# Optimization experiments

Hardware: AMD Instinct MI355X
Metric: run time of the kernel (lower is better)

The kernel has to match this reference:

```python
import jax, jax.numpy as jnp
import numpy as np

N_USER = 200000
N_TITEM = 200000  # sized >= N_USER because original code indexes ti_emb with user ids (faithful to source bug)
D = 256           # embed_dim
H = 128           # hidden = embed_dim // 2
N_HID = 2         # config.layers - 1 extra hidden blocks
B = 65536


def setup_inputs() -> dict:
    key = jax.random.key(0)
    ks = jax.random.split(key, 10)
    sc_d = 1.0 / np.sqrt(D)
    sc_h = 1.0 / np.sqrt(H)
    return {
        "user": jax.random.randint(ks[0], (B,), 0, N_USER),
        "item": jax.random.randint(ks[1], (B,), 0, 100000),
        "su_table": jax.random.normal(ks[2], (N_USER, D), jnp.float32) * 0.1,
        "ti_table": jax.random.normal(ks[3], (N_TITEM, D), jnp.float32) * 0.1,
        # 3 parallel MLP towers, stacked on leading axis t=3
        "Win": jax.random.normal(ks[4], (3, D, H), jnp.float32) * sc_d,
        "bin_": jnp.zeros((3, H), jnp.float32),
        "Wh": jax.random.normal(ks[5], (3, N_HID, H, H), jnp.float32) * sc_h,
        "bh": jnp.zeros((3, N_HID, H), jnp.float32),
        "Wout": jax.random.normal(ks[6], (3, H, D), jnp.float32) * sc_h,
        "bout": jnp.zeros((3, D), jnp.float32),
    }


def _towers(u, Win, bin_, Wh, bh, Wout, bout):
    # u: [B, D] -> x: [3, B, D] (three structurally identical MLP towers, batched)
    h = jax.nn.relu(jnp.einsum("bd,tdh->tbh", u, Win) + bin_[:, None, :])
    for i in range(N_HID):  # fixed small layer count
        h = jax.nn.relu(jnp.einsum("tbh,thk->tbk", h, Wh[:, i]) + bh[:, i][:, None, :])
    return jnp.einsum("tbh,thd->tbd", h, Wout) + bout[:, None, :]


def reference(user, item, su_table, ti_table, Win, bin_, Wh, bh, Wout, bout):
    u_embed = su_table[user]            # [B, D]
    i_key = ti_table[user]              # [B, D]  (faithful: original indexes ti_emb with `user`)
    x = _towers(u_embed, Win, bin_, Wh, bh, Wout, bout)   # [3, B, D]
    logits = jnp.einsum("tbd,bd->bt", x, i_key)           # [B, 3]
    attn = jax.nn.softmax(logits, axis=1)                 # [B, 3]
    fu = jnp.einsum("bt,tbd->bd", attn, x)                # [B, D]
    i_embed = ti_table[item]                              # [B, D]
    score = jnp.sum(fu * i_embed, axis=1)                 # [B]
    return score
```

## Files before the change

kernel.cpp:

```cpp
#include <hip/hip_runtime.h>
#include <hip/hip_bf16.h>
#include <stdint.h>

typedef __attribute__((ext_vector_type(8))) short short8;
typedef __attribute__((ext_vector_type(4))) float f32x4;

__device__ __forceinline__ short f2bf(float f) {
  __hip_bfloat16 h = __float2bfloat16(f);
  union { __hip_bfloat16 h; unsigned short u; } c;
  c.h = h;
  return (short)c.u;
}
__device__ __forceinline__ short8 cvt8(const float* p) {
  const float4 f0 = *(const float4*)p;
  const float4 f1 = *(const float4*)(p + 4);
  short8 r;
  r[0] = f2bf(f0.x); r[1] = f2bf(f0.y); r[2] = f2bf(f0.z); r[3] = f2bf(f0.w);
  r[4] = f2bf(f1.x); r[5] = f2bf(f1.y); r[6] = f2bf(f1.z); r[7] = f2bf(f1.w);
  return r;
}

__global__ __launch_bounds__(256) void pack_weights(
    const float* __restrict__ Win, const float* __restrict__ Wh,
    const float* __restrict__ Wout, short* __restrict__ o) {
  int gid = blockIdx.x * 256 + threadIdx.x;
  if (gid < 12288) {
    int t = gid / 4096, r = gid % 4096;
    int ks = r / 512, r2 = r % 512, nf = r2 / 64, l = r2 % 64;
    int n = nf * 16 + (l & 15);
    int kb = ks * 32 + (l >> 4) * 8;
#pragma unroll
    for (int i = 0; i < 8; ++i)
      o[gid * 8 + i] = f2bf(Win[(t * 256 + kb + i) * 128 + n]);
  } else if (gid < 24576) {
    int h = gid - 12288;
    int tl = h / 2048, r = h % 2048;
    int ks = r / 512, nf = (r % 512) / 64, l = r % 64;
    int n = nf * 16 + (l & 15);
    int kb = ks * 32 + (l >> 4) * 8;
#pragma unroll
    for (int i = 0; i < 8; ++i)
      o[98304 + h * 8 + i] = f2bf(Wh[(tl * 128 + kb + i) * 128 + n]);
  } else {
    int oo = gid - 24576;
    int t = oo / 4096, r = oo % 4096;
    int ks = r / 1024, nf = (r % 1024) / 64, l = r % 64;
    int n = nf * 16 + (l & 15);
    int kb = ks * 32 + (l >> 4) * 8;
#pragma unroll
    for (int i = 0; i < 8; ++i)
      o[196608 + oo * 8 + i] = f2bf(Wout[(t * 128 + kb + i) * 256 + n]);
  }
}

__device__ __forceinline__ void stageN(const short* __restrict__ wp, char* lbuf,
                                       int pageBase, int tid, int rounds) {
  const char* g = (const char*)wp + (size_t)pageBase * 1024 + (size_t)tid * 16;
  char* l = lbuf + (tid >> 6) * 1024;
  for (int r = 0; r < rounds; ++r) {
    __builtin_amdgcn_global_load_lds(
        (const __attribute__((address_space(1))) void*)(g + r * 4096),
        (__attribute__((address_space(3))) void*)(l + r * 4096), 16, 0, 0);
  }
}

__global__ __launch_bounds__(256) void k_gather_u(
    const int* __restrict__ user, const float* __restrict__ su,
    short* __restrict__ U, int nrows) {
  const int idx = blockIdx.x * 256 + threadIdx.x;
  const int row = idx >> 5, c = idx & 31;
  const int uid = user[row];
  *(short8*)(U + (size_t)row * 256 + c * 8) = cvt8(su + (size_t)uid * 256 + c * 8);
}

__global__ __launch_bounds__(256, 2) void k_l1(
    const short* __restrict__ U, const float* __restrict__ bin,
    const short* __restrict__ wp, short* __restrict__ H1, int nrows) {
  __shared__ __align__(16) char sB[65536];
  const int tid = threadIdx.x, w = tid >> 6, lane = tid & 63;
  const int ar = lane & 15, g = lane >> 4;
  const int t = blockIdx.y;
  const int rblk = blockIdx.x * 128;
  const f32x4 fz = {0.f, 0.f, 0.f, 0.f};

  stageN(wp, sB, t * 64, tid, 16);
  __syncthreads();

  f32x4 acc[8][2];
#pragma unroll
  for (int m = 0; m < 8; ++m) { acc[m][0] = fz; acc[m][1] = fz; }
#pragma unroll
  for (int K0 = 0; K0 < 8; ++K0) {
    short8 a[8];
#pragma unroll
    for (int m = 0; m < 8; ++m)
      a[m] = *(const short8*)(U + (size_t)(rblk + m * 16 + ar) * 256 + K0 * 32 + g * 8);
#pragma unroll
    for (int nfl = 0; nfl < 2; ++nfl) {
      const short8 b = *(const short8*)(sB + (K0 * 8 + w * 2 + nfl) * 1024 + lane * 16);
#pragma unroll
      for (int m = 0; m < 8; ++m)
        acc[m][nfl] = __builtin_amdgcn_mfma_f32_16x16x32_bf16(a[m], b, acc[m][nfl], 0, 0, 0);
    }
  }
#pragma unroll
  for (int m = 0; m < 8; ++m)
#pragma unroll
    for (int nfl = 0; nfl < 2; ++nfl) {
      const int col = w * 32 + nfl * 16 + ar;
      const float bv = bin[t * 128 + col];
#pragma unroll
      for (int q = 0; q < 4; ++q) {
        const int r = rblk + m * 16 + g * 4 + q;
        H1[((size_t)t * nrows + r) * 128 + col] = f2bf(fmaxf(acc[m][nfl][q] + bv, 0.f));
      }
    }
}

__global__ __launch_bounds__(256, 2) void k_l23(
    const short* __restrict__ H1, const float* __restrict__ bh,
    const short* __restrict__ wp, short* __restrict__ H3, int nrows) {
  __shared__ __align__(16) char sB[65536];
  __shared__ __align__(16) char H2[16384];
  const int tid = threadIdx.x, w = tid >> 6, lane = tid & 63;
  const int ar = lane & 15, g = lane >> 4;
  const int t = blockIdx.y;
  const int rblk = blockIdx.x * 64;
  const int swzA = (ar & 7) << 4;
  const f32x4 fz = {0.f, 0.f, 0.f, 0.f};

  stageN(wp, sB, 192 + t * 64, tid, 16);
  __syncthreads();

  f32x4 acc[4][2];
#pragma unroll
  for (int m = 0; m < 4; ++m) { acc[m][0] = fz; acc[m][1] = fz; }
#pragma unroll
  for (int ks = 0; ks < 4; ++ks) {
    short8 a[4];
#pragma unroll
    for (int m = 0; m < 4; ++m)
      a[m] = *(const short8*)(H1 + ((size_t)t * nrows + rblk + m * 16 + ar) * 128 + ks * 32 + g * 8);
#pragma unroll
    for (int nfl = 0; nfl < 2; ++nfl) {
      const short8 b = *(const short8*)(sB + (ks * 8 + w * 2 + nfl) * 1024 + lane * 16);
#pragma unroll
      for (int m = 0; m < 4; ++m)
        acc[m][nfl] = __builtin_amdgcn_mfma_f32_16x16x32_bf16(a[m], b, acc[m][nfl], 0, 0, 0);
    }
  }
#pragma unroll
  for (int m = 0; m < 4; ++m)
#pragma unroll
    for (int nfl = 0; nfl < 2; ++nfl) {
      const int col = w * 32 + nfl * 16 + ar;
      const float bv = bh[(t * 2) * 128 + col];
#pragma unroll
      for (int q = 0; q < 4; ++q) {
        const int r = m * 16 + g * 4 + q;
        *(short*)(H2 + r * 256 + ((col * 2) ^ ((r & 7) << 4))) =
            f2bf(fmaxf(acc[m][nfl][q] + bv, 0.f));
      }
    }
  __syncthreads();

#pragma unroll
  for (int m = 0; m < 4; ++m) { acc[m][0] = fz; acc[m][1] = fz; }
#pragma unroll
  for (int ks = 0; ks < 4; ++ks) {
    short8 a[4];
#pragma unroll
    for (int m = 0; m < 4; ++m)
      a[m] = *(const short8*)(H2 + (m * 16 + ar) * 256 + ((ks * 64 + g * 16) ^ swzA));
#pragma unroll
    for (int nfl = 0; nfl < 2; ++nfl) {
      const short8 b = *(const short8*)(sB + (32 + ks * 8 + w * 2 + nfl) * 1024 + lane * 16);
#pragma unroll
      for (int m = 0; m < 4; ++m)
        acc[m][nfl] = __builtin_amdgcn_mfma_f32_16x16x32_bf16(a[m], b, acc[m][nfl], 0, 0, 0);
    }
  }
#pragma unroll
  for (int m = 0; m < 4; ++m)
#pragma unroll
    for (int nfl = 0; nfl < 2; ++nfl) {
      const int col = w * 32 + nfl * 16 + ar;
      const float bv = bh[(t * 2 + 1) * 128 + col];
#pragma unroll
      for (int q = 0; q < 4; ++q) {
        const int r = rblk + m * 16 + g * 4 + q;
        H3[((size_t)t * nrows + r) * 128 + col] = f2bf(fmaxf(acc[m][nfl][q] + bv, 0.f));
      }
    }
}

__global__ __launch_bounds__(256, 2) void k_l4tail(
    const short* __restrict__ H3, const float* __restrict__ bout,
    const short* __restrict__ wp, const float* __restrict__ ti,
    const int* __restrict__ user, const int* __restrict__ item,
    float* __restrict__ out, int nrows) {
  __shared__ __align__(16) char WB[2][32768];
  __shared__ float sL[3][64];
  __shared__ float sS[3][64];
  __shared__ int sUid[64];
  __shared__ int sItm[64];
  const int tid = threadIdx.x, w = tid >> 6, lane = tid & 63;
  const int ar = lane & 15, g = lane >> 4;
  const int rblk = blockIdx.x * 64;
  const f32x4 fz = {0.f, 0.f, 0.f, 0.f};

  if (tid < 64) {
    sUid[tid] = user[rblk + tid];
    sItm[tid] = item[rblk + tid];
  }
  if (tid < 192) { (&sL[0][0])[tid] = 0.f; (&sS[0][0])[tid] = 0.f; }
  stageN(wp, WB[0], 384, tid, 8);
  __syncthreads();
  int cur = 0;

  for (int t = 0; t < 3; ++t) {
    f32x4 acc4[4][4];
#pragma unroll
    for (int m = 0; m < 4; ++m)
#pragma unroll
      for (int n = 0; n < 4; ++n) acc4[m][n] = fz;

    for (int half = 0; half < 2; ++half) {
      const int phase = t * 2 + half;
      if (phase < 5) stageN(wp, WB[cur ^ 1], 384 + (phase + 1) * 32, tid, 8);
      const char* wb = WB[cur];
#pragma unroll
      for (int k2 = 0; k2 < 2; ++k2) {
        const int K0 = half * 2 + k2;
        short8 a[4];
#pragma unroll
        for (int m = 0; m < 4; ++m)
          a[m] = *(const short8*)(H3 + ((size_t)t * nrows + rblk + m * 16 + ar) * 128 + K0 * 32 + g * 8);
#pragma unroll
        for (int nfl = 0; nfl < 4; ++nfl) {
          const short8 b = *(const short8*)(wb + (k2 * 16 + w * 4 + nfl) * 1024 + lane * 16);
#pragma unroll
          for (int m = 0; m < 4; ++m)
            acc4[m][nfl] = __builtin_amdgcn_mfma_f32_16x16x32_bf16(a[m], b, acc4[m][nfl], 0, 0, 0);
        }
      }

      if (half == 1) {
        float pl[16], ps[16];
#pragma unroll
        for (int i = 0; i < 16; ++i) { pl[i] = 0.f; ps[i] = 0.f; }
#pragma unroll
        for (int m = 0; m < 4; ++m)
#pragma unroll
          for (int nfl = 0; nfl < 4; ++nfl) {
            const int col = w * 64 + nfl * 16 + ar;
            const float bo = bout[t * 256 + col];
#pragma unroll
            for (int q = 0; q < 4; ++q) {
              const int r = m * 16 + g * 4 + q;
              const float x = acc4[m][nfl][q] + bo;
              pl[m * 4 + q] += x * ti[(size_t)sUid[r] * 256 + col];
              ps[m * 4 + q] += x * ti[(size_t)sItm[r] * 256 + col];
            }
          }
#pragma unroll
        for (int i = 0; i < 16; ++i) {
          float a0 = pl[i], b0 = ps[i];
#pragma unroll
          for (int off = 1; off < 16; off <<= 1) {
            a0 += __shfl_xor(a0, off);
            b0 += __shfl_xor(b0, off);
          }
          pl[i] = a0; ps[i] = b0;
        }
        if (ar == 0) {
#pragma unroll
          for (int m = 0; m < 4; ++m)
#pragma unroll
            for (int q = 0; q < 4; ++q) {
              const int r = m * 16 + g * 4 + q;
              atomicAdd(&sL[t][r], pl[m * 4 + q]);
              atomicAdd(&sS[t][r], ps[m * 4 + q]);
            }
        }
      }
      __syncthreads();
      cur ^= 1;
    }
  }

  if (tid < 64) {
    const float l0 = sL[0][tid], l1 = sL[1][tid], l2 = sL[2][tid];
    const float mx = fmaxf(l0, fmaxf(l1, l2));
    const float e0 = __expf(l0 - mx), e1 = __expf(l1 - mx), e2 = __expf(l2 - mx);
    out[rblk + tid] =
        (e0 * sS[0][tid] + e1 * sS[1][tid] + e2 * sS[2][tid]) / (e0 + e1 + e2);
  }
}

extern "C" void kernel_launch(void* const* d_in, const int* in_sizes, int n_in,
                              void* d_out, int out_size, void* d_ws, size_t ws_size,
                              hipStream_t stream) {
  const int* user = (const int*)d_in[0];
  const int* item = (const int*)d_in[1];
  const float* su = (const float*)d_in[2];
  const float* ti = (const float*)d_in[3];
  const float* Win = (const float*)d_in[4];
  const float* bin = (const float*)d_in[5];
  const float* Wh = (const float*)d_in[6];
  const float* bh = (const float*)d_in[7];
  const float* Wout = (const float*)d_in[8];
  const float* bout = (const float*)d_in[9];
  float* out = (float*)d_out;
  char* ws = (char*)d_ws;

  const size_t WOFF = 1179648;
  short* wpk = (short*)ws;
  hipLaunchKernelGGL(pack_weights, dim3(144), dim3(256), 0, stream, Win, Wh, Wout, wpk);

  size_t avail = (ws_size > WOFF) ? (ws_size - WOFF) : 0;
  long rpc = (long)((avail / 2048) & ~(size_t)127);
  if (rpc > 65536) rpc = 65536;
  if (rpc < 128) rpc = 128;

  short* U = (short*)(ws + WOFF);
  short* H1 = (short*)(ws + WOFF + (size_t)rpc * 512);
  short* H3 = (short*)(ws + WOFF + (size_t)rpc * 512 + (size_t)rpc * 768);

  for (long r0 = 0; r0 < 65536; r0 += rpc) {
    const int nr = (int)((65536 - r0 < rpc) ? (65536 - r0) : rpc);
    hipLaunchKernelGGL(k_gather_u, dim3(nr / 8), dim3(256), 0, stream,
                       user + r0, su, U, nr);
    hipLaunchKernelGGL(k_l1, dim3(nr / 128, 3), dim3(256), 0, stream,
                       U, bin, wpk, H1, nr);
    hipLaunchKernelGGL(k_l23, dim3(nr / 64, 3), dim3(256), 0, stream,
                       H1, bh, wpk, H3, nr);
    hipLaunchKernelGGL(k_l4tail, dim3(nr / 64), dim3(256), 0, stream,
                       H3, bout, wpk, ti, user + r0, item + r0, out + r0, nr);
  }
}
```

Measured before the change: 204.7 us.

## Use persistent grid-stride GEMM kernels and split the output layer from the attention tail

The layer kernels become persistent, capped at 170 blocks per tower, and loop over row tiles, so each block stages its 64KB weight slice into LDS once and reuses it. k_l23 is restructured so each wave owns 16 rows with a private LDS slab, which removes the block-wide barrier between layers 2 and 3. The fused l4+tail kernel is split into a per-tower output GEMM that writes bf16 X to a workspace, followed by a separate vectorized tail kernel that does the ti gathers, dot products and softmax. This adds a [3,B,256] bf16 intermediate round-trip through global memory, and the larger per-row footprint may lower rows per chunk when workspace is small.

```diff
diff --git a/kernel.cpp b/kernel.cpp
--- a/kernel.cpp
+++ b/kernel.cpp
@@ -10,6 +10,10 @@
   union { __hip_bfloat16 h; unsigned short u; } c;
   c.h = h;
   return (short)c.u;
+}
+__device__ __forceinline__ float bf2f(short s) {
+  union { unsigned u; float f; } x; x.u = ((unsigned)(unsigned short)s) << 16;
+  return x.f;
 }
 __device__ __forceinline__ short8 cvt8(const float* p) {
   const float4 f0 = *(const float4*)p;
@@ -80,41 +84,44 @@
   const int tid = threadIdx.x, w = tid >> 6, lane = tid & 63;
   const int ar = lane & 15, g = lane >> 4;
   const int t = blockIdx.y;
-  const int rblk = blockIdx.x * 128;
   const f32x4 fz = {0.f, 0.f, 0.f, 0.f};
 
   stageN(wp, sB, t * 64, tid, 16);
   __syncthreads();
 
-  f32x4 acc[8][2];
-#pragma unroll
-  for (int m = 0; m < 8; ++m) { acc[m][0] = fz; acc[m][1] = fz; }
-#pragma unroll
-  for (int K0 = 0; K0 < 8; ++K0) {
-    short8 a[8];
+  const int ntile = nrows >> 7;
+  for (int tile = blockIdx.x; tile < ntile; tile += gridDim.x) {
+    const int rblk = tile << 7;
+    f32x4 acc[8][2];
+#pragma unroll
+    for (int m = 0; m < 8; ++m) { acc[m][0] = fz; acc[m][1] = fz; }
+#pragma unroll
+    for (int K0 = 0; K0 < 8; ++K0) {
+      short8 a[8];
+#pragma unroll
+      for (int m = 0; m < 8; ++m)
+        a[m] = *(const short8*)(U + (size_t)(rblk + m * 16 + ar) * 256 + K0 * 32 + g * 8);
+#pragma unroll
+      for (int nfl = 0; nfl < 2; ++nfl) {
+        const short8 b = *(const short8*)(sB + (K0 * 8 + w * 2 + nfl) * 1024 + lane * 16);
+#pragma unroll
+        for (int m = 0; m < 8; ++m)
+          acc[m][nfl] = __builtin_amdgcn_mfma_f32_16x16x32_bf16(a[m], b, acc[m][nfl], 0, 0, 0);
+      }
+    }
 #pragma unroll
     for (int m = 0; m < 8; ++m)
-      a[m] = *(const short8*)(U + (size_t)(rblk + m * 16 + ar) * 256 + K0 * 32 + g * 8);
-#pragma unroll
-    for (int nfl = 0; nfl < 2; ++nfl) {
-      const short8 b = *(const short8*)(sB + (K0 * 8 + w * 2 + nfl) * 1024 + lane * 16);
-#pragma unroll
-      for (int m = 0; m < 8; ++m)
-        acc[m][nfl] = __builtin_amdgcn_mfma_f32_16x16x32_bf16(a[m], b, acc[m][nfl], 0, 0, 0);
-    }
-  }
-#pragma unroll
-  for (int m = 0; m < 8; ++m)
-#pragma unroll
-    for (int nfl = 0; nfl < 2; ++nfl) {
-      const int col = w * 32 + nfl * 16 + ar;
-      const float bv = bin[t * 128 + col];
-#pragma unroll
-      for (int q = 0; q < 4; ++q) {
-        const int r = rblk + m * 16 + g * 4 + q;
-        H1[((size_t)t * nrows + r) * 128 + col] = f2bf(fmaxf(acc[m][nfl][q] + bv, 0.f));
-      }
-    }
+#pragma unroll
+      for (int nfl = 0; nfl < 2; ++nfl) {
+        const int col = w * 32 + nfl * 16 + ar;
+        const float bv = bin[t * 128 + col];
+#pragma unroll
+        for (int q = 0; q < 4; ++q) {
+          const int r = rblk + m * 16 + g * 4 + q;
+          H1[((size_t)t * nrows + r) * 128 + col] = f2bf(fmaxf(acc[m][nfl][q] + bv, 0.f));
+        }
+      }
+  }
 }
 
 __global__ __launch_bounds__(256, 2) void k_l23(
@@ -125,176 +132,150 @@
   const int tid = threadIdx.x, w = tid >> 6, lane = tid & 63;
   const int ar = lane & 15, g = lane >> 4;
   const int t = blockIdx.y;
-  const int rblk = blockIdx.x * 64;
   const int swzA = (ar & 7) << 4;
   const f32x4 fz = {0.f, 0.f, 0.f, 0.f};
 
   stageN(wp, sB, 192 + t * 64, tid, 16);
   __syncthreads();
 
-  f32x4 acc[4][2];
-#pragma unroll
-  for (int m = 0; m < 4; ++m) { acc[m][0] = fz; acc[m][1] = fz; }
-#pragma unroll
-  for (int ks = 0; ks < 4; ++ks) {
-    short8 a[4];
-#pragma unroll
-    for (int m = 0; m < 4; ++m)
-      a[m] = *(const short8*)(H1 + ((size_t)t * nrows + rblk + m * 16 + ar) * 128 + ks * 32 + g * 8);
-#pragma unroll
-    for (int nfl = 0; nfl < 2; ++nfl) {
-      const short8 b = *(const short8*)(sB + (ks * 8 + w * 2 + nfl) * 1024 + lane * 16);
-#pragma unroll
-      for (int m = 0; m < 4; ++m)
-        acc[m][nfl] = __builtin_amdgcn_mfma_f32_16x16x32_bf16(a[m], b, acc[m][nfl], 0, 0, 0);
-    }
-  }
-#pragma unroll
-  for (int m = 0; m < 4; ++m)
-#pragma unroll
-    for (int nfl = 0; nfl < 2; ++nfl) {
-      const int col = w * 32 + nfl * 16 + ar;
+  char* const h2 = H2 + w * 4096;
+  const int ntile = nrows >> 6;
+  for (int tile = blockIdx.x; tile < ntile; tile += gridDim.x) {
+    const int base = tile * 64 + w * 16;
+    f32x4 acc[8];
+#pragma unroll
+    for (int nf = 0; nf < 8; ++nf) acc[nf] = fz;
+#pragma unroll
+    for (int ks = 0; ks < 4; ++ks) {
+      const short8 a = *(const short8*)(H1 + ((size_t)t * nrows + base + ar) * 128 + ks * 32 + g * 8);
+#pragma unroll
+      for (int nf = 0; nf < 8; ++nf) {
+        const short8 b = *(const short8*)(sB + (ks * 8 + nf) * 1024 + lane * 16);
+        acc[nf] = __builtin_amdgcn_mfma_f32_16x16x32_bf16(a, b, acc[nf], 0, 0, 0);
+      }
+    }
+#pragma unroll
+    for (int nf = 0; nf < 8; ++nf) {
+      const int col = nf * 16 + ar;
       const float bv = bh[(t * 2) * 128 + col];
 #pragma unroll
       for (int q = 0; q < 4; ++q) {
-        const int r = m * 16 + g * 4 + q;
-        *(short*)(H2 + r * 256 + ((col * 2) ^ ((r & 7) << 4))) =
-            f2bf(fmaxf(acc[m][nfl][q] + bv, 0.f));
-      }
-    }
+        const int r = g * 4 + q;
+        *(short*)(h2 + r * 256 + ((col * 2) ^ ((r & 7) << 4))) =
+            f2bf(fmaxf(acc[nf][q] + bv, 0.f));
+      }
+    }
+#pragma unroll
+    for (int nf = 0; nf < 8; ++nf) acc[nf] = fz;
+#pragma unroll
+    for (int ks = 0; ks < 4; ++ks) {
+      const short8 a = *(const short8*)(h2 + ar * 256 + ((ks * 64 + g * 16) ^ swzA));
+#pragma unroll
+      for (int nf = 0; nf < 8; ++nf) {
+        const short8 b = *(const short8*)(sB + (32 + ks * 8 + nf) * 1024 + lane * 16);
+        acc[nf] = __builtin_amdgcn_mfma_f32_16x16x32_bf16(a, b, acc[nf], 0, 0, 0);
+      }
+    }
+#pragma unroll
+    for (int nf = 0; nf < 8; ++nf) {
+      const int col = nf * 16 + ar;
+      const float bv = bh[(t * 2 + 1) * 128 + col];
+#pragma unroll
+      for (int q = 0; q < 4; ++q) {
+        const int r = base + g * 4 + q;
+        H3[((size_t)t * nrows + r) * 128 + col] = f2bf(fmaxf(acc[nf][q] + bv, 0.f));
+      }
+    }
+  }
+}
+
+__global__ __launch_bounds__(256, 2) void k_l4(
+    const short* __restrict__ H3, const float* __restrict__ bout,
+    const short* __restrict__ wp, short* __restrict__ X, int nrows) {
+  __shared__ __align__(16) char sB[65536];
+  const int tid = threadIdx.x, w = tid >> 6, lane = tid & 63;
+  const int ar = lane & 15, g = lane >> 4;
+  const int t = blockIdx.y;
+  const f32x4 fz = {0.f, 0.f, 0.f, 0.f};
+
+  stageN(wp, sB, 384 + t * 64, tid, 16);
   __syncthreads();
 
-#pragma unroll
-  for (int m = 0; m < 4; ++m) { acc[m][0] = fz; acc[m][1] = fz; }
-#pragma unroll
-  for (int ks = 0; ks < 4; ++ks) {
-    short8 a[4];
-#pragma unroll
-    for (int m = 0; m < 4; ++m)
-      a[m] = *(const short8*)(H2 + (m * 16 + ar) * 256 + ((ks * 64 + g * 16) ^ swzA));
-#pragma unroll
-    for (int nfl = 0; nfl < 2; ++nfl) {
-      const short8 b = *(const short8*)(sB + (32 + ks * 8 + w * 2 + nfl) * 1024 + lane * 16);
-#pragma unroll
-      for (int m = 0; m < 4; ++m)
-        acc[m][nfl] = __builtin_amdgcn_mfma_f32_16x16x32_bf16(a[m], b, acc[m][nfl], 0, 0, 0);
-    }
-  }
-#pragma unroll
-  for (int m = 0; m < 4; ++m)
-#pragma unroll
-    for (int nfl = 0; nfl < 2; ++nfl) {
-      const int col = w * 32 + nfl * 16 + ar;
-      const float bv = bh[(t * 2 + 1) * 128 + col];
+  float bo[16];
+#pragma unroll
+  for (int nf = 0; nf < 16; ++nf) bo[nf] = bout[t * 256 + nf * 16 + ar];
+
+  const int ntile = nrows >> 6;
+  for (int tile = blockIdx.x; tile < ntile; tile += gridDim.x) {
+    const int base = tile * 64 + w * 16;
+    short8 a4[4];
+#pragma unroll
+    for (int K0 = 0; K0 < 4; ++K0)
+      a4[K0] = *(const short8*)(H3 + ((size_t)t * nrows + base + ar) * 128 + K0 * 32 + g * 8);
+    f32x4 acc[16];
+#pragma unroll
+    for (int nf = 0; nf < 16; ++nf) acc[nf] = fz;
+#pragma unroll
+    for (int K0 = 0; K0 < 4; ++K0)
+#pragma unroll
+      for (int nf = 0; nf < 16; ++nf) {
+        const short8 b = *(const short8*)(sB + (K0 * 16 + nf) * 1024 + lane * 16);
+        acc[nf] = __builtin_amdgcn_mfma_f32_16x16x32_bf16(a4[K0], b, acc[nf], 0, 0, 0);
+      }
+#pragma unroll
+    for (int nf = 0; nf < 16; ++nf) {
+      const int col = nf * 16 + ar;
 #pragma unroll
       for (int q = 0; q < 4; ++q) {
-        const int r = rblk + m * 16 + g * 4 + q;
-        H3[((size_t)t * nrows + r) * 128 + col] = f2bf(fmaxf(acc[m][nfl][q] + bv, 0.f));
-      }
-    }
-}
-
-__global__ __launch_bounds__(256, 2) void k_l4tail(
-    const short* __restrict__ H3, const float* __restrict__ bout,
-    const short* __restrict__ wp, const float* __restrict__ ti,
+        const int r = base + g * 4 + q;
+        X[((size_t)t * nrows + r) * 256 + col] = f2bf(acc[nf][q] + bo[nf]);
+      }
+    }
+  }
+}
+
+__global__ __launch_bounds__(256) void k_tail(
+    const short* __restrict__ X, const float* __restrict__ ti,
     const int* __restrict__ user, const int* __restrict__ item,
     float* __restrict__ out, int nrows) {
-  __shared__ __align__(16) char WB[2][32768];
-  __shared__ float sL[3][64];
-  __shared__ float sS[3][64];
-  __shared__ int sUid[64];
-  __shared__ int sItm[64];
-  const int tid = threadIdx.x, w = tid >> 6, lane = tid & 63;
-  const int ar = lane & 15, g = lane >> 4;
-  const int rblk = blockIdx.x * 64;
-  const f32x4 fz = {0.f, 0.f, 0.f, 0.f};
-
-  if (tid < 64) {
-    sUid[tid] = user[rblk + tid];
-    sItm[tid] = item[rblk + tid];
-  }
-  if (tid < 192) { (&sL[0][0])[tid] = 0.f; (&sS[0][0])[tid] = 0.f; }
-  stageN(wp, WB[0], 384, tid, 8);
-  __syncthreads();
-  int cur = 0;
-
-  for (int t = 0; t < 3; ++t) {
-    f32x4 acc4[4][4];
-#pragma unroll
-    for (int m = 0; m < 4; ++m)
-#pragma unroll
-      for (int n = 0; n < 4; ++n) acc4[m][n] = fz;
-
-    for (int half = 0; half < 2; ++half) {
-      const int phase = t * 2 + half;
-      if (phase < 5) stageN(wp, WB[cur ^ 1], 384 + (phase + 1) * 32, tid, 8);
-      const char* wb = WB[cur];
-#pragma unroll
-      for (int k2 = 0; k2 < 2; ++k2) {
-        const int K0 = half * 2 + k2;
-        short8 a[4];
-#pragma unroll
-        for (int m = 0; m < 4; ++m)
-          a[m] = *(const short8*)(H3 + ((size_t)t * nrows + rblk + m * 16 + ar) * 128 + K0 * 32 + g * 8);
-#pragma unroll
-        for (int nfl = 0; nfl < 4; ++nfl) {
-          const short8 b = *(const short8*)(wb + (k2 * 16 + w * 4 + nfl) * 1024 + lane * 16);
-#pragma unroll
-          for (int m = 0; m < 4; ++m)
-            acc4[m][nfl] = __builtin_amdgcn_mfma_f32_16x16x32_bf16(a[m], b, acc4[m][nfl], 0, 0, 0);
-        }
-      }
-
-      if (half == 1) {
-        float pl[16], ps[16];
-#pragma unroll
-        for (int i = 0; i < 16; ++i) { pl[i] = 0.f; ps[i] = 0.f; }
-#pragma unroll
-        for (int m = 0; m < 4; ++m)
-#pragma unroll
-          for (int nfl = 0; nfl < 4; ++nfl) {
-            const int col = w * 64 + nfl * 16 + ar;
-            const float bo = bout[t * 256 + col];
-#pragma unroll
-            for (int q = 0; q < 4; ++q) {
-              const int r = m * 16 + g * 4 + q;
-              const float x = acc4[m][nfl][q] + bo;
-              pl[m * 4 + q] += x * ti[(size_t)sUid[r] * 256 + col];
-              ps[m * 4 + q] += x * ti[(size_t)sItm[r] * 256 + col];
-            }
-          }
-#pragma unroll
-        for (int i = 0; i < 16; ++i) {
-          float a0 = pl[i], b0 = ps[i];
-#pragma unroll
-          for (int off = 1; off < 16; off <<= 1) {
-            a0 += __shfl_xor(a0, off);
-            b0 += __shfl_xor(b0, off);
-          }
-          pl[i] = a0; ps[i] = b0;
-        }
-        if (ar == 0) {
-#pragma unroll
-          for (int m = 0; m < 4; ++m)
-#pragma unroll
-            for (int q = 0; q < 4; ++q) {
-              const int r = m * 16 + g * 4 + q;
-              atomicAdd(&sL[t][r], pl[m * 4 + q]);
-              atomicAdd(&sS[t][r], ps[m * 4 + q]);
-            }
-        }
-      }
-      __syncthreads();
-      cur ^= 1;
-    }
-  }
-
-  if (tid < 64) {
-    const float l0 = sL[0][tid], l1 = sL[1][tid], l2 = sL[2][tid];
+  const int tid = threadIdx.x;
+  const int rr = tid >> 2, qq = tid & 3;
+  const int row = blockIdx.x * 64 + rr;
+  const int uid = user[row], itm = item[row];
+  const float* kv = ti + (size_t)uid * 256 + qq * 64;
+  const float* ev = ti + (size_t)itm * 256 + qq * 64;
+
+  float l0 = 0.f, l1 = 0.f, l2 = 0.f, s0 = 0.f, s1 = 0.f, s2 = 0.f;
+#pragma unroll
+  for (int i = 0; i < 8; ++i) {
+    const float4 ka = *(const float4*)(kv + i * 8);
+    const float4 kb = *(const float4*)(kv + i * 8 + 4);
+    const float4 ea = *(const float4*)(ev + i * 8);
+    const float4 eb = *(const float4*)(ev + i * 8 + 4);
+#pragma unroll
+    for (int t = 0; t < 3; ++t) {
+      const short8 xv = *(const short8*)(X + ((size_t)t * nrows + row) * 256 + qq * 64 + i * 8);
+      const float x0 = bf2f(xv[0]), x1 = bf2f(xv[1]), x2 = bf2f(xv[2]), x3 = bf2f(xv[3]);
+      const float x4 = bf2f(xv[4]), x5 = bf2f(xv[5]), x6 = bf2f(xv[6]), x7 = bf2f(xv[7]);
+      const float dl = x0 * ka.x + x1 * ka.y + x2 * ka.z + x3 * ka.w
+                     + x4 * kb.x + x5 * kb.y + x6 * kb.z + x7 * kb.w;
+      const float ds = x0 * ea.x + x1 * ea.y + x2 * ea.z + x3 * ea.w
+                     + x4 * eb.x + x5 * eb.y + x6 * eb.z + x7 * eb.w;
+      if (t == 0) { l0 += dl; s0 += ds; }
+      else if (t == 1) { l1 += dl; s1 += ds; }
+      else { l2 += dl; s2 += ds; }
+    }
+  }
+  l0 += __shfl_xor(l0, 1); l0 += __shfl_xor(l0, 2);
+  l1 += __shfl_xor(l1, 1); l1 += __shfl_xor(l1, 2);
+  l2 += __shfl_xor(l2, 1); l2 += __shfl_xor(l2, 2);
+  s0 += __shfl_xor(s0, 1); s0 += __shfl_xor(s0, 2);
+  s1 += __shfl_xor(s1, 1); s1 += __shfl_xor(s1, 2);
+  s2 += __shfl_xor(s2, 1); s2 += __shfl_xor(s2, 2);
+  if (qq == 0) {
     const float mx = fmaxf(l0, fmaxf(l1, l2));
     const float e0 = __expf(l0 - mx), e1 = __expf(l1 - mx), e2 = __expf(l2 - mx);
-    out[rblk + tid] =
-        (e0 * sS[0][tid] + e1 * sS[1][tid] + e2 * sS[2][tid]) / (e0 + e1 + e2);
+    out[row] = (e0 * s0 + e1 * s1 + e2 * s2) / (e0 + e1 + e2);
   }
 }
 
@@ -319,23 +300,25 @@
   hipLaunchKernelGGL(pack_weights, dim3(144), dim3(256), 0, stream, Win, Wh, Wout, wpk);
 
   size_t avail = (ws_size > WOFF) ? (ws_size - WOFF) : 0;
-  long rpc = (long)((avail / 2048) & ~(size_t)127);
+  long rpc = (long)((avail / 3584) & ~(size_t)127);
   if (rpc > 65536) rpc = 65536;
   if (rpc < 128) rpc = 128;
 
   short* U = (short*)(ws + WOFF);
   short* H1 = (short*)(ws + WOFF + (size_t)rpc * 512);
-  short* H3 = (short*)(ws + WOFF + (size_t)rpc * 512 + (size_t)rpc * 768);
+  short* H3 = (short*)(ws + WOFF + (size_t)rpc * 1280);
+  short* X = (short*)(ws + WOFF + (size_t)rpc * 2048);
 
   for (long r0 = 0; r0 < 65536; r0 += rpc) {
     const int nr = (int)((65536 - r0 < rpc) ? (65536 - r0) : rpc);
+    const int g1 = (nr / 128 < 170) ? (nr / 128) : 170;
+    const int g2 = (nr / 64 < 170) ? (nr / 64) : 170;
     hipLaunchKernelGGL(k_gather_u, dim3(nr / 8), dim3(256), 0, stream,
                        user + r0, su, U, nr);
-    hipLaunchKernelGGL(k_l1, dim3(nr / 128, 3), dim3(256), 0, stream,
-                       U, bin, wpk, H1, nr);
-    hipLaunchKernelGGL(k_l23, dim3(nr / 64, 3), dim3(256), 0, stream,
-                       H1, bh, wpk, H3, nr);
-    hipLaunchKernelGGL(k_l4tail, dim3(nr / 64), dim3(256), 0, stream,
-                       H3, bout, wpk, ti, user + r0, item + r0, out + r0, nr);
-  }
-}
+    hipLaunchKernelGGL(k_l1, dim3(g1, 3), dim3(256), 0, stream, U, bin, wpk, H1, nr);
+    hipLaunchKernelGGL(k_l23, dim3(g2, 3), dim3(256), 0, stream, H1, bh, wpk, H3, nr);
+    hipLaunchKernelGGL(k_l4, dim3(g2, 3), dim3(256), 0, stream, H3, bout, wpk, X, nr);
+    hipLaunchKernelGGL(k_tail, dim3(nr / 64), dim3(256), 0, stream,
+                       X, ti, user + r0, item + r0, out + r0, nr);
+  }
+}
```

Result: slower. 405.6 us (+98.2%).
